# Kernel optimization log

Hardware: AMD Instinct MI355X
Metric: run time of the kernel (lower is better)

Reference implementation:

```python
import jax, jax.numpy as jnp
import numpy as np

D_MODEL = 1024
N_HEADS = 16
B, T = 2, 2048


def setup_inputs() -> dict:
    key = jax.random.key(0)
    kx, kqkv, ko = jax.random.split(key, 3)
    x = jax.random.normal(kx, (B, T, D_MODEL), dtype=jnp.float32)
    # flax Linear default init (lecun_normal ~ scaled); plain scaled normal is fine for a baseline
    Wqkv = jax.random.normal(kqkv, (D_MODEL, 3 * D_MODEL), dtype=jnp.float32) / np.sqrt(D_MODEL)
    Wo = jax.random.normal(ko, (D_MODEL, D_MODEL), dtype=jnp.float32) / np.sqrt(D_MODEL)
    return {"x": x, "Wqkv": Wqkv, "Wo": Wo}


def reference(x, Wqkv, Wo):
    Bx, Tx, C = x.shape
    H = N_HEADS
    Hd = C // H
    scale = C ** (-0.5)  # NOTE: module scales by d_model**-0.5, not head_dim**-0.5
    qkv = x @ Wqkv  # [B, T, 3C]
    q, k, v = jnp.split(qkv, 3, axis=-1)
    q = q.reshape(Bx, Tx, H, Hd).transpose(0, 2, 1, 3)  # [B,H,T,Hd]
    k = k.reshape(Bx, Tx, H, Hd).transpose(0, 2, 1, 3)
    v = v.reshape(Bx, Tx, H, Hd).transpose(0, 2, 1, 3)
    attn = jnp.einsum('bhid,bhjd->bhij', q, k) * scale  # [B,H,T,T]
    mask = jnp.tril(jnp.ones((Tx, Tx), dtype=jnp.bool_))
    attn = jnp.where(mask[None, None], attn, jnp.finfo(attn.dtype).min)
    attn = jax.nn.softmax(attn.astype(jnp.float32), axis=-1).astype(attn.dtype)
    out = jnp.einsum('bhij,bhjd->bhid', attn, v)  # [B,H,T,Hd]
    out = out.transpose(0, 2, 1, 3).reshape(Bx, Tx, C)
    return out @ Wo
```

## Files before the change

### kernel.cpp

```cpp
#include <hip/hip_runtime.h>
#include <cstdint>
#include <math.h>

#define D_MODEL 1024
#define N_HEADS 16
#define HEAD_DIM 64
#define BB 2
#define TT 2048
#define QSCALE 0.04508422002778011f
#define MSTATIC 12.0f

typedef float f32x4 __attribute__((ext_vector_type(4)));
typedef __bf16 bf16x8 __attribute__((ext_vector_type(8)));

__device__ inline ushort f2bf(float f) {
    union { float f; uint32_t u; } c; c.f = f;
    uint32_t u = c.u;
    uint32_t r = (u + 0x7FFFu + ((u >> 16) & 1u)) >> 16;
    return (ushort)r;
}
__device__ inline ushort f2bf_hw(float f) {
    __bf16 h = (__bf16)f;
    return __builtin_bit_cast(ushort, h);
}

__device__ inline void load_lds16(const ushort* g, ushort* lds_uniform_base) {
    __builtin_amdgcn_global_load_lds(
        (const __attribute__((address_space(1))) uint32_t*)g,
        (__attribute__((address_space(3))) uint32_t*)lds_uniform_base, 16, 0, 0);
}

__global__ __launch_bounds__(256) void prep(
    const float4* __restrict__ xin, ushort4* __restrict__ xb,
    const float* __restrict__ Wqkv, ushort* __restrict__ WqkvT,
    const float* __restrict__ Wo, ushort* __restrict__ WoT)
{
    int bid = blockIdx.x;
    int tid = threadIdx.x;
    if (bid < 4096) {
        int i = bid * 256 + tid;
        float4 v = xin[i];
        ushort4 u;
        u.x = f2bf(v.x); u.y = f2bf(v.y); u.z = f2bf(v.z); u.w = f2bf(v.w);
        xb[i] = u;
        return;
    }
    __shared__ ushort tile[32][33];
    int tx = tid & 31, ty = tid >> 5;
    const float* in; ushort* out; int R, C, c0, r0;
    if (bid < 7168) {
        int b2 = bid - 4096;
        in = Wqkv; out = WqkvT; R = D_MODEL; C = 3 * D_MODEL;
        c0 = (b2 % 96) * 32; r0 = (b2 / 96) * 32;
    } else {
        int b3 = bid - 7168;
        in = Wo; out = WoT; R = D_MODEL; C = D_MODEL;
        c0 = (b3 % 32) * 32; r0 = (b3 / 32) * 32;
    }
#pragma unroll
    for (int i = 0; i < 32; i += 8)
        tile[ty + i][tx] = f2bf(in[(size_t)(r0 + ty + i) * C + (c0 + tx)]);
    __syncthreads();
#pragma unroll
    for (int i = 0; i < 32; i += 8)
        out[(size_t)(c0 + ty + i) * R + (r0 + tx)] = tile[tx][ty + i];
}

__global__ __launch_bounds__(256) void transpose_v_bf16(
    const ushort* __restrict__ in, ushort* __restrict__ out)
{
    int z = blockIdx.z;
    const ushort* ip = in + (size_t)z * TT * HEAD_DIM;
    ushort* op = out + (size_t)z * TT * HEAD_DIM;
    __shared__ ushort tile[32][33];
    int tx = threadIdx.x, ty = threadIdx.y;
    int d0 = blockIdx.x * 32;
    int t0 = blockIdx.y * 32;
#pragma unroll
    for (int i = 0; i < 32; i += 8)
        tile[ty + i][tx] = ip[(size_t)(t0 + ty + i) * HEAD_DIM + d0 + tx];
    __syncthreads();
#pragma unroll
    for (int i = 0; i < 32; i += 8)
        op[(size_t)(d0 + ty + i) * TT + t0 + tx] = tile[tx][ty + i];
}

__device__ inline void gemm128_mainloop(
    const ushort* __restrict__ A, const ushort* __restrict__ BT,
    int rowBase, int colBase, ushort* Al, ushort* Bl,
    f32x4 acc[4][4], int wave, int lane)
{
    const int K = D_MODEL;
    int lr = lane & 15, quad = lane >> 4;
    int lrow = lane >> 2;
    int kq = lane & 3;
    int mq = (wave >> 1) * 64, nq = (wave & 1) * 64;

    const ushort* gA0 = A + (size_t)(rowBase + wave * 32 + lrow) * K + kq * 8;
    const ushort* gA1 = gA0 + (size_t)16 * K;
    const ushort* gB0 = BT + (size_t)(colBase + wave * 32 + lrow) * K + kq * 8;
    const ushort* gB1 = gB0 + (size_t)16 * K;
    ushort* lA0 = Al + (wave * 32) * 32;
    ushort* lA1 = Al + (wave * 32 + 16) * 32;
    ushort* lB0 = Bl + (wave * 32) * 32;
    ushort* lB1 = Bl + (wave * 32 + 16) * 32;

    for (int kt = 0; kt < K / 32; ++kt) {
        __syncthreads();
        int ko = kt * 32;
        load_lds16(gA0 + ko, lA0);
        load_lds16(gA1 + ko, lA1);
        load_lds16(gB0 + ko, lB0);
        load_lds16(gB1 + ko, lB1);
        __syncthreads();
        bf16x8 af[4], bf[4];
#pragma unroll
        for (int mi = 0; mi < 4; ++mi)
            af[mi] = *(const bf16x8*)(Al + (mq + mi * 16 + lr) * 32 + quad * 8);
#pragma unroll
        for (int ni = 0; ni < 4; ++ni)
            bf[ni] = *(const bf16x8*)(Bl + (nq + ni * 16 + lr) * 32 + quad * 8);
#pragma unroll
        for (int mi = 0; mi < 4; ++mi)
#pragma unroll
            for (int ni = 0; ni < 4; ++ni)
                acc[mi][ni] = __builtin_amdgcn_mfma_f32_16x16x32_bf16(
                    af[mi], bf[ni], acc[mi][ni], 0, 0, 0);
    }
}

__global__ __launch_bounds__(256) void gemm_qkv(
    const ushort* __restrict__ A, const ushort* __restrict__ BT,
    ushort* __restrict__ Qo, ushort* __restrict__ Ko, ushort* __restrict__ Vo)
{
    __shared__ ushort Al[128 * 32];
    __shared__ ushort Bl[128 * 32];
    int tid = threadIdx.x;
    int wave = tid >> 6, lane = tid & 63;
    int lr = lane & 15, quad = lane >> 4;
    int rowBase = blockIdx.y * 128;
    int colBase = blockIdx.x * 128;
    f32x4 acc[4][4] = {};
    gemm128_mainloop(A, BT, rowBase, colBase, Al, Bl, acc, wave, lane);

    int mq = (wave >> 1) * 64, nq = (wave & 1) * 64;
#pragma unroll
    for (int ni = 0; ni < 4; ++ni) {
        int n = colBase + nq + ni * 16 + lr;
        int s = n >> 10;
        int cc = n & 1023;
        int h = cc >> 6, d = cc & 63;
        ushort* dst = (s == 0) ? Qo : (s == 1 ? Ko : Vo);
        float scale = (s == 0) ? QSCALE : 1.0f;
#pragma unroll
        for (int mi = 0; mi < 4; ++mi) {
#pragma unroll
            for (int i = 0; i < 4; ++i) {
                int m = rowBase + mq + mi * 16 + quad * 4 + i;
                int b = m >> 11, t = m & 2047;
                int bh = b * N_HEADS + h;
                dst[((size_t)bh * TT + t) * HEAD_DIM + d] = f2bf(acc[mi][ni][i] * scale);
            }
        }
    }
}

__global__ __launch_bounds__(256) void gemm_plain(
    const ushort* __restrict__ A, const ushort* __restrict__ BT,
    float* __restrict__ O, int N)
{
    const int K = D_MODEL;
    __shared__ ushort Al[128 * 32];
    __shared__ ushort Bl[64 * 32];
    int tid = threadIdx.x;
    int wave = tid >> 6, lane = tid & 63;
    int lr = lane & 15, quad = lane >> 4;
    int lrow = lane >> 2, kq = lane & 3;
    int rowBase = blockIdx.y * 128;
    int colBase = blockIdx.x * 64;
    int mq = (wave >> 1) * 64, nq = (wave & 1) * 32;

    const ushort* gA0 = A + (size_t)(rowBase + wave * 32 + lrow) * K + kq * 8;
    const ushort* gA1 = gA0 + (size_t)16 * K;
    const ushort* gB0 = BT + (size_t)(colBase + wave * 32 + lrow) * K + kq * 8;
    const ushort* gB1 = gB0 + (size_t)16 * K;
    ushort* lA0 = Al + (wave * 32) * 32;
    ushort* lA1 = Al + (wave * 32 + 16) * 32;
    ushort* lB0 = Bl + (wave * 32) * 32;
    ushort* lB1 = Bl + (wave * 32 + 16) * 32;

    f32x4 acc[4][2] = {};
    for (int kt = 0; kt < K / 32; ++kt) {
        __syncthreads();
        int ko = kt * 32;
        load_lds16(gA0 + ko, lA0);
        load_lds16(gA1 + ko, lA1);
        if (wave < 2) {
            load_lds16(gB0 + ko, lB0);
            load_lds16(gB1 + ko, lB1);
        }
        __syncthreads();
        bf16x8 af[4], bf[2];
#pragma unroll
        for (int mi = 0; mi < 4; ++mi)
            af[mi] = *(const bf16x8*)(Al + (mq + mi * 16 + lr) * 32 + quad * 8);
#pragma unroll
        for (int ni = 0; ni < 2; ++ni)
            bf[ni] = *(const bf16x8*)(Bl + (nq + ni * 16 + lr) * 32 + quad * 8);
#pragma unroll
        for (int mi = 0; mi < 4; ++mi)
#pragma unroll
            for (int ni = 0; ni < 2; ++ni)
                acc[mi][ni] = __builtin_amdgcn_mfma_f32_16x16x32_bf16(
                    af[mi], bf[ni], acc[mi][ni], 0, 0, 0);
    }

#pragma unroll
    for (int mi = 0; mi < 4; ++mi)
#pragma unroll
        for (int ni = 0; ni < 2; ++ni) {
            int n = colBase + nq + ni * 16 + lr;
#pragma unroll
            for (int i = 0; i < 4; ++i) {
                int m = rowBase + mq + mi * 16 + quad * 4 + i;
                O[(size_t)m * N + n] = acc[mi][ni][i];
            }
        }
}

__global__ __launch_bounds__(256) void attn_flash(
    const ushort* __restrict__ Q,
    const ushort* __restrict__ K,
    const ushort* __restrict__ VT,
    ushort* __restrict__ AO)
{
    int bid = blockIdx.x;
    int xcd  = bid & 7;
    int slot = bid >> 3;
    int bh   = (slot >> 4) * 8 + xcd;
    int idx  = slot & 15;
    int tid = threadIdx.x;
    int wave = tid >> 6, lane = tid & 63;
    int quad = lane >> 4, lr = lane & 15;

    int a    = idx * 4 + wave;
    int Gl   = a;
    int Gh   = 127 - a;
    int rowl = Gl << 4;
    int rowh = Gh << 4;
    int liml = Gl >> 1;
    int limh = Gh >> 1;
    int bt64 = 32 - idx;

    const ushort* Qb = Q  + (size_t)bh * TT * HEAD_DIM;
    const ushort* Kb = K  + (size_t)bh * TT * HEAD_DIM;
    const ushort* Vb = VT + (size_t)bh * HEAD_DIM * TT;

    __shared__ ushort Kl[2][8 * 64 * 8];
    __shared__ ushort Vl[2][8 * 64 * 8];
    __shared__ ushort pbuf[4][32][40];
    ushort (*P)[40] = pbuf[wave];

    const ushort* gK0 = Kb + (size_t)lane * HEAD_DIM + wave * 8;
    const ushort* gK1 = Kb + (size_t)lane * HEAD_DIM + (wave + 4) * 8;
    const ushort* gV0 = Vb + (size_t)lane * TT + wave * 8;
    const ushort* gV1 = Vb + (size_t)lane * TT + 32 + wave * 8;

    bf16x8 qa[2][2];
#pragma unroll
    for (int r = 0; r < 2; ++r) {
        int rb = (r == 0) ? rowl : rowh;
#pragma unroll
        for (int s = 0; s < 2; ++s)
            qa[r][s] = *(const bf16x8*)(Qb + (size_t)(rb + lr) * HEAD_DIM
                                           + s * 32 + quad * 8);
    }

    f32x4 o[2][4] = {};
    f32x4 l[2] = {};

    bf16x8 ones;
#pragma unroll
    for (int j = 0; j < 8; ++j) ones[j] = (__bf16)1.0f;

    load_lds16(gK0, Kl[0] + wave * 512);
    load_lds16(gK1, Kl[0] + (wave + 4) * 512);
    load_lds16(gV0, Vl[0] + wave * 512);
    load_lds16(gV1, Vl[0] + (wave + 4) * 512);
    __syncthreads();

    for (int kt64 = 0; kt64 < bt64; ++kt64) {
        int cur = kt64 & 1;
        if (kt64 + 1 < bt64) {
            size_t koff = (size_t)(kt64 + 1) * 64;
            ushort* KlN = Kl[cur ^ 1];
            ushort* VlN = Vl[cur ^ 1];
            load_lds16(gK0 + koff * HEAD_DIM, KlN + wave * 512);
            load_lds16(gK1 + koff * HEAD_DIM, KlN + (wave + 4) * 512);
            load_lds16(gV0 + koff, VlN + wave * 512);
            load_lds16(gV1 + koff, VlN + (wave + 4) * 512);
        }
        const ushort* Klc = Kl[cur];
        const ushort* Vlc = Vl[cur];

#pragma unroll
        for (int sub = 0; sub < 2; ++sub) {
            int kt32 = kt64 * 2 + sub;
            if (kt32 > limh) break;
            int act0 = (kt32 <= liml);

            bf16x8 kb[2][2];
#pragma unroll
            for (int c = 0; c < 2; ++c)
#pragma unroll
                for (int s = 0; s < 2; ++s)
                    kb[c][s] = *(const bf16x8*)&Klc[(((s * 4 + quad) * 64)
                                 + sub * 32 + c * 16 + lr) * 8];
            bf16x8 vb[4];
#pragma unroll
            for (int d = 0; d < 4; ++d)
                vb[d] = *(const bf16x8*)&Vlc[(((sub * 4 + quad) * 64)
                             + d * 16 + lr) * 8];

#pragma unroll
            for (int r = 0; r < 2; ++r) {
                if (r == 0 && !act0) continue;
                int rb  = (r == 0) ? rowl : rowh;
                int lim = (r == 0) ? liml : limh;

                f32x4 sc[2];
#pragma unroll
                for (int c = 0; c < 2; ++c)
#pragma unroll
                    for (int i = 0; i < 4; ++i) sc[c][i] = -MSTATIC;
#pragma unroll
                for (int c = 0; c < 2; ++c) {
                    sc[c] = __builtin_amdgcn_mfma_f32_16x16x32_bf16(kb[c][0], qa[r][0], sc[c], 0, 0, 0);
                    sc[c] = __builtin_amdgcn_mfma_f32_16x16x32_bf16(kb[c][1], qa[r][1], sc[c], 0, 0, 0);
                }
                if (kt32 == lim) {
#pragma unroll
                    for (int c = 0; c < 2; ++c)
#pragma unroll
                        for (int i = 0; i < 4; ++i)
                            if (kt32 * 32 + c * 16 + quad * 4 + i > rb + lr)
                                sc[c][i] = -3e38f;
                }
#pragma unroll
                for (int c = 0; c < 2; ++c) {
                    uint2 pk;
                    pk.x = (uint32_t)f2bf_hw(__builtin_amdgcn_exp2f(sc[c][0]))
                         | ((uint32_t)f2bf_hw(__builtin_amdgcn_exp2f(sc[c][1])) << 16);
                    pk.y = (uint32_t)f2bf_hw(__builtin_amdgcn_exp2f(sc[c][2]))
                         | ((uint32_t)f2bf_hw(__builtin_amdgcn_exp2f(sc[c][3])) << 16);
                    *(uint2*)&P[r * 16 + lr][c * 16 + quad * 4] = pk;
                }
            }

#pragma unroll
            for (int r = 0; r < 2; ++r) {
                if (r == 0 && !act0) continue;
                bf16x8 pa = *(const bf16x8*)&P[r * 16 + lr][quad * 8];
                l[r] = __builtin_amdgcn_mfma_f32_16x16x32_bf16(pa, ones, l[r], 0, 0, 0);
#pragma unroll
                for (int d = 0; d < 4; ++d)
                    o[r][d] = __builtin_amdgcn_mfma_f32_16x16x32_bf16(pa, vb[d], o[r][d], 0, 0, 0);
            }
        }
        __syncthreads();
    }

    int b = bh >> 4, h = bh & 15;
#pragma unroll
    for (int r = 0; r < 2; ++r) {
        int rb = (r == 0) ? rowl : rowh;
        f32x4 rl;
#pragma unroll
        for (int i = 0; i < 4; ++i) rl[i] = 1.0f / l[r][i];
#pragma unroll
        for (int d = 0; d < 4; ++d)
#pragma unroll
            for (int i = 0; i < 4; ++i) {
                int row = rb + quad * 4 + i;
                AO[((size_t)(b * TT + row)) * D_MODEL + h * HEAD_DIM + d * 16 + lr] =
                    f2bf(o[r][d][i] * rl[i]);
            }
    }
}

extern "C" void kernel_launch(void* const* d_in, const int* in_sizes, int n_in,
                              void* d_out, int out_size, void* d_ws, size_t ws_size,
                              hipStream_t stream)
{
    (void)in_sizes; (void)n_in; (void)out_size; (void)ws_size;
    const float* x    = (const float*)d_in[0];
    const float* Wqkv = (const float*)d_in[1];
    const float* Wo   = (const float*)d_in[2];
    float* out = (float*)d_out;

    char* ws = (char*)d_ws;
    size_t off = 0;
    ushort* WqkvT = (ushort*)(ws + off); off += (size_t)3 * D_MODEL * D_MODEL * 2;
    ushort* WoT   = (ushort*)(ws + off); off += (size_t)D_MODEL * D_MODEL * 2;
    ushort* xb    = (ushort*)(ws + off); off += (size_t)BB * TT * D_MODEL * 2;
    ushort* Qd    = (ushort*)(ws + off); off += (size_t)BB * D_MODEL * TT * 2;
    ushort* Kd    = (ushort*)(ws + off); off += (size_t)BB * D_MODEL * TT * 2;
    ushort* Vd    = (ushort*)(ws + off); off += (size_t)BB * D_MODEL * TT * 2;
    ushort* VTd   = (ushort*)(ws + off); off += (size_t)BB * D_MODEL * TT * 2;
    ushort* AO    = (ushort*)(ws + off); off += (size_t)BB * TT * D_MODEL * 2;

    prep<<<dim3(8192), 256, 0, stream>>>(
        (const float4*)x, (ushort4*)xb, Wqkv, WqkvT, Wo, WoT);

    gemm_qkv<<<dim3(3 * D_MODEL / 128, BB * TT / 128), 256, 0, stream>>>(
        xb, WqkvT, Qd, Kd, Vd);

    transpose_v_bf16<<<dim3(HEAD_DIM / 32, TT / 32, BB * N_HEADS), dim3(32, 8), 0, stream>>>(
        Vd, VTd);

    attn_flash<<<dim3(512), 256, 0, stream>>>(Qd, Kd, VTd, AO);

    gemm_plain<<<dim3(D_MODEL / 64, BB * TT / 128), 256, 0, stream>>>(
        AO, WoT, out, D_MODEL);
}
```

Baseline: 193.6 us.

## Fuse V transpose into attention kernel via register-staged transposed LDS writes

```diff
diff --git a/kernel.cpp b/kernel.cpp
--- a/kernel.cpp
+++ b/kernel.cpp
@@ -28,6 +28,16 @@
     __builtin_amdgcn_global_load_lds(
         (const __attribute__((address_space(1))) uint32_t*)g,
         (__attribute__((address_space(3))) uint32_t*)lds_uniform_base, 16, 0, 0);
+}
+
+__device__ inline void vwrite(ushort* Vbuf, int row, int chk, uint4 v, int lane) {
+    const ushort* e = (const ushort*)&v;
+    int base = (row >> 3) * 512 + (row & 7);
+#pragma unroll
+    for (int jj = 0; jj < 8; ++jj) {
+        int j = (jj + (lane & 7)) & 7;
+        Vbuf[base + (chk * 8 + j) * 8] = e[j];
+    }
 }
 
 __global__ __launch_bounds__(256) void prep(
@@ -66,25 +76,6 @@
         out[(size_t)(c0 + ty + i) * R + (r0 + tx)] = tile[tx][ty + i];
 }
 
-__global__ __launch_bounds__(256) void transpose_v_bf16(
-    const ushort* __restrict__ in, ushort* __restrict__ out)
-{
-    int z = blockIdx.z;
-    const ushort* ip = in + (size_t)z * TT * HEAD_DIM;
-    ushort* op = out + (size_t)z * TT * HEAD_DIM;
-    __shared__ ushort tile[32][33];
-    int tx = threadIdx.x, ty = threadIdx.y;
-    int d0 = blockIdx.x * 32;
-    int t0 = blockIdx.y * 32;
-#pragma unroll
-    for (int i = 0; i < 32; i += 8)
-        tile[ty + i][tx] = ip[(size_t)(t0 + ty + i) * HEAD_DIM + d0 + tx];
-    __syncthreads();
-#pragma unroll
-    for (int i = 0; i < 32; i += 8)
-        op[(size_t)(d0 + ty + i) * TT + t0 + tx] = tile[tx][ty + i];
-}
-
 __device__ inline void gemm128_mainloop(
     const ushort* __restrict__ A, const ushort* __restrict__ BT,
     int rowBase, int colBase, ushort* Al, ushort* Bl,
@@ -231,7 +222,7 @@
 __global__ __launch_bounds__(256) void attn_flash(
     const ushort* __restrict__ Q,
     const ushort* __restrict__ K,
-    const ushort* __restrict__ VT,
+    const ushort* __restrict__ V,
     ushort* __restrict__ AO)
 {
     int bid = blockIdx.x;
@@ -252,9 +243,9 @@
     int limh = Gh >> 1;
     int bt64 = 32 - idx;
 
-    const ushort* Qb = Q  + (size_t)bh * TT * HEAD_DIM;
-    const ushort* Kb = K  + (size_t)bh * TT * HEAD_DIM;
-    const ushort* Vb = VT + (size_t)bh * HEAD_DIM * TT;
+    const ushort* Qb = Q + (size_t)bh * TT * HEAD_DIM;
+    const ushort* Kb = K + (size_t)bh * TT * HEAD_DIM;
+    const ushort* Vb = V + (size_t)bh * TT * HEAD_DIM;
 
     __shared__ ushort Kl[2][8 * 64 * 8];
     __shared__ ushort Vl[2][8 * 64 * 8];
@@ -263,8 +254,8 @@
 
     const ushort* gK0 = Kb + (size_t)lane * HEAD_DIM + wave * 8;
     const ushort* gK1 = Kb + (size_t)lane * HEAD_DIM + (wave + 4) * 8;
-    const ushort* gV0 = Vb + (size_t)lane * TT + wave * 8;
-    const ushort* gV1 = Vb + (size_t)lane * TT + 32 + wave * 8;
+    int vrow = tid >> 3;
+    int vchk = tid & 7;
 
     bf16x8 qa[2][2];
 #pragma unroll
@@ -283,22 +274,28 @@
 #pragma unroll
     for (int j = 0; j < 8; ++j) ones[j] = (__bf16)1.0f;
 
+    {
+        uint4 v0 = *(const uint4*)(Vb + (size_t)vrow * HEAD_DIM + vchk * 8);
+        uint4 v1 = *(const uint4*)(Vb + (size_t)(vrow + 32) * HEAD_DIM + vchk * 8);
+        vwrite(Vl[0], vrow, vchk, v0, lane);
+        vwrite(Vl[0], vrow + 32, vchk, v1, lane);
+    }
     load_lds16(gK0, Kl[0] + wave * 512);
     load_lds16(gK1, Kl[0] + (wave + 4) * 512);
-    load_lds16(gV0, Vl[0] + wave * 512);
-    load_lds16(gV1, Vl[0] + (wave + 4) * 512);
     __syncthreads();
 
     for (int kt64 = 0; kt64 < bt64; ++kt64) {
         int cur = kt64 & 1;
-        if (kt64 + 1 < bt64) {
+        uint4 nv0, nv1;
+        int pf = (kt64 + 1 < bt64);
+        if (pf) {
             size_t koff = (size_t)(kt64 + 1) * 64;
+            const ushort* vs = Vb + koff * HEAD_DIM;
+            nv0 = *(const uint4*)(vs + (size_t)vrow * HEAD_DIM + vchk * 8);
+            nv1 = *(const uint4*)(vs + (size_t)(vrow + 32) * HEAD_DIM + vchk * 8);
             ushort* KlN = Kl[cur ^ 1];
-            ushort* VlN = Vl[cur ^ 1];
             load_lds16(gK0 + koff * HEAD_DIM, KlN + wave * 512);
             load_lds16(gK1 + koff * HEAD_DIM, KlN + (wave + 4) * 512);
-            load_lds16(gV0 + koff, VlN + wave * 512);
-            load_lds16(gV1 + koff, VlN + (wave + 4) * 512);
         }
         const ushort* Klc = Kl[cur];
         const ushort* Vlc = Vl[cur];
@@ -366,6 +363,10 @@
                 for (int d = 0; d < 4; ++d)
                     o[r][d] = __builtin_amdgcn_mfma_f32_16x16x32_bf16(pa, vb[d], o[r][d], 0, 0, 0);
             }
+        }
+        if (pf) {
+            vwrite(Vl[cur ^ 1], vrow, vchk, nv0, lane);
+            vwrite(Vl[cur ^ 1], vrow + 32, vchk, nv1, lane);
         }
         __syncthreads();
     }
@@ -408,6 +409,7 @@
     ushort* Vd    = (ushort*)(ws + off); off += (size_t)BB * D_MODEL * TT * 2;
     ushort* VTd   = (ushort*)(ws + off); off += (size_t)BB * D_MODEL * TT * 2;
     ushort* AO    = (ushort*)(ws + off); off += (size_t)BB * TT * D_MODEL * 2;
+    (void)VTd;
 
     prep<<<dim3(8192), 256, 0, stream>>>(
         (const float4*)x, (ushort4*)xb, Wqkv, WqkvT, Wo, WoT);
@@ -415,10 +417,7 @@
     gemm_qkv<<<dim3(3 * D_MODEL / 128, BB * TT / 128), 256, 0, stream>>>(
         xb, WqkvT, Qd, Kd, Vd);
 
-    transpose_v_bf16<<<dim3(HEAD_DIM / 32, TT / 32, BB * N_HEADS), dim3(32, 8), 0, stream>>>(
-        Vd, VTd);
-
-    attn_flash<<<dim3(512), 256, 0, stream>>>(Qd, Kd, VTd, AO);
+    attn_flash<<<dim3(512), 256, 0, stream>>>(Qd, Kd, Vd, AO);
 
     gemm_plain<<<dim3(D_MODEL / 64, BB * TT / 128), 256, 0, stream>>>(
         AO, WoT, out, D_MODEL);
```

After: 213.5 us. 10.3% more time.

## Double-buffer LDS tiles in QKV and output projection GEMMs

Applied to the files above, without the earlier changes.

```diff
diff --git a/kernel.cpp b/kernel.cpp
--- a/kernel.cpp
+++ b/kernel.cpp
@@ -100,32 +100,42 @@
     const ushort* gA1 = gA0 + (size_t)16 * K;
     const ushort* gB0 = BT + (size_t)(colBase + wave * 32 + lrow) * K + kq * 8;
     const ushort* gB1 = gB0 + (size_t)16 * K;
-    ushort* lA0 = Al + (wave * 32) * 32;
-    ushort* lA1 = Al + (wave * 32 + 16) * 32;
-    ushort* lB0 = Bl + (wave * 32) * 32;
-    ushort* lB1 = Bl + (wave * 32 + 16) * 32;
+    int oS0 = (wave * 32) * 32;
+    int oS1 = (wave * 32 + 16) * 32;
+
+    load_lds16(gA0, Al + oS0);
+    load_lds16(gA1, Al + oS1);
+    load_lds16(gB0, Bl + oS0);
+    load_lds16(gB1, Bl + oS1);
+    __syncthreads();
 
     for (int kt = 0; kt < K / 32; ++kt) {
-        __syncthreads();
-        int ko = kt * 32;
-        load_lds16(gA0 + ko, lA0);
-        load_lds16(gA1 + ko, lA1);
-        load_lds16(gB0 + ko, lB0);
-        load_lds16(gB1 + ko, lB1);
-        __syncthreads();
+        int cur = kt & 1;
+        if (kt + 1 < K / 32) {
+            int ko = (kt + 1) * 32;
+            ushort* AlN = Al + (cur ^ 1) * 4096;
+            ushort* BlN = Bl + (cur ^ 1) * 4096;
+            load_lds16(gA0 + ko, AlN + oS0);
+            load_lds16(gA1 + ko, AlN + oS1);
+            load_lds16(gB0 + ko, BlN + oS0);
+            load_lds16(gB1 + ko, BlN + oS1);
+        }
+        const ushort* Alc = Al + cur * 4096;
+        const ushort* Blc = Bl + cur * 4096;
         bf16x8 af[4], bf[4];
 #pragma unroll
         for (int mi = 0; mi < 4; ++mi)
-            af[mi] = *(const bf16x8*)(Al + (mq + mi * 16 + lr) * 32 + quad * 8);
+            af[mi] = *(const bf16x8*)(Alc + (mq + mi * 16 + lr) * 32 + quad * 8);
 #pragma unroll
         for (int ni = 0; ni < 4; ++ni)
-            bf[ni] = *(const bf16x8*)(Bl + (nq + ni * 16 + lr) * 32 + quad * 8);
+            bf[ni] = *(const bf16x8*)(Blc + (nq + ni * 16 + lr) * 32 + quad * 8);
 #pragma unroll
         for (int mi = 0; mi < 4; ++mi)
 #pragma unroll
             for (int ni = 0; ni < 4; ++ni)
                 acc[mi][ni] = __builtin_amdgcn_mfma_f32_16x16x32_bf16(
                     af[mi], bf[ni], acc[mi][ni], 0, 0, 0);
+        __syncthreads();
     }
 }
 
@@ -133,15 +143,15 @@
     const ushort* __restrict__ A, const ushort* __restrict__ BT,
     ushort* __restrict__ Qo, ushort* __restrict__ Ko, ushort* __restrict__ Vo)
 {
-    __shared__ ushort Al[128 * 32];
-    __shared__ ushort Bl[128 * 32];
+    __shared__ ushort Al[2][128 * 32];
+    __shared__ ushort Bl[2][128 * 32];
     int tid = threadIdx.x;
     int wave = tid >> 6, lane = tid & 63;
     int lr = lane & 15, quad = lane >> 4;
     int rowBase = blockIdx.y * 128;
     int colBase = blockIdx.x * 128;
     f32x4 acc[4][4] = {};
-    gemm128_mainloop(A, BT, rowBase, colBase, Al, Bl, acc, wave, lane);
+    gemm128_mainloop(A, BT, rowBase, colBase, Al[0], Bl[0], acc, wave, lane);
 
     int mq = (wave >> 1) * 64, nq = (wave & 1) * 64;
 #pragma unroll
@@ -170,8 +180,8 @@
     float* __restrict__ O, int N)
 {
     const int K = D_MODEL;
-    __shared__ ushort Al[128 * 32];
-    __shared__ ushort Bl[64 * 32];
+    __shared__ ushort Al[2][128 * 32];
+    __shared__ ushort Bl[2][64 * 32];
     int tid = threadIdx.x;
     int wave = tid >> 6, lane = tid & 63;
     int lr = lane & 15, quad = lane >> 4;
@@ -184,35 +194,45 @@
     const ushort* gA1 = gA0 + (size_t)16 * K;
     const ushort* gB0 = BT + (size_t)(colBase + wave * 32 + lrow) * K + kq * 8;
     const ushort* gB1 = gB0 + (size_t)16 * K;
-    ushort* lA0 = Al + (wave * 32) * 32;
-    ushort* lA1 = Al + (wave * 32 + 16) * 32;
-    ushort* lB0 = Bl + (wave * 32) * 32;
-    ushort* lB1 = Bl + (wave * 32 + 16) * 32;
+    int oS0 = (wave * 32) * 32;
+    int oS1 = (wave * 32 + 16) * 32;
+
+    load_lds16(gA0, Al[0] + oS0);
+    load_lds16(gA1, Al[0] + oS1);
+    if (wave < 2) {
+        load_lds16(gB0, Bl[0] + oS0);
+        load_lds16(gB1, Bl[0] + oS1);
+    }
+    __syncthreads();
 
     f32x4 acc[4][2] = {};
     for (int kt = 0; kt < K / 32; ++kt) {
-        __syncthreads();
-        int ko = kt * 32;
-        load_lds16(gA0 + ko, lA0);
-        load_lds16(gA1 + ko, lA1);
-        if (wave < 2) {
-            load_lds16(gB0 + ko, lB0);
-            load_lds16(gB1 + ko, lB1);
-        }
-        __syncthreads();
+        int cur = kt & 1;
+        if (kt + 1 < K / 32) {
+            int ko = (kt + 1) * 32;
+            load_lds16(gA0 + ko, Al[cur ^ 1] + oS0);
+            load_lds16(gA1 + ko, Al[cur ^ 1] + oS1);
+            if (wave < 2) {
+                load_lds16(gB0 + ko, Bl[cur ^ 1] + oS0);
+                load_lds16(gB1 + ko, Bl[cur ^ 1] + oS1);
+            }
+        }
+        const ushort* Alc = Al[cur];
+        const ushort* Blc = Bl[cur];
         bf16x8 af[4], bf[2];
 #pragma unroll
         for (int mi = 0; mi < 4; ++mi)
-            af[mi] = *(const bf16x8*)(Al + (mq + mi * 16 + lr) * 32 + quad * 8);
+            af[mi] = *(const bf16x8*)(Alc + (mq + mi * 16 + lr) * 32 + quad * 8);
 #pragma unroll
         for (int ni = 0; ni < 2; ++ni)
-            bf[ni] = *(const bf16x8*)(Bl + (nq + ni * 16 + lr) * 32 + quad * 8);
+            bf[ni] = *(const bf16x8*)(Blc + (nq + ni * 16 + lr) * 32 + quad * 8);
 #pragma unroll
         for (int mi = 0; mi < 4; ++mi)
 #pragma unroll
             for (int ni = 0; ni < 2; ++ni)
                 acc[mi][ni] = __builtin_amdgcn_mfma_f32_16x16x32_bf16(
                     af[mi], bf[ni], acc[mi][ni], 0, 0, 0);
+        __syncthreads();
     }
 
 #pragma unroll
```

New measurement: 191.5 us. About the same (-1.1%).
